# Kernel optimization log

Measured on AMD Instinct MI355X. Metric: run time of the kernel, lower is better.

The kernel has to match this reference:

```python
import jax, jax.numpy as jnp
import numpy as np

B, T, C, H, N, FF = 2, 1024, 2048, 32, 64, 8192
DIV = 8.0  # head_size_divisor
LAYER_ID, N_LAYER = 1, 24
EPS = 1e-5


def _layer_norm(x, g, b):
    m = x.mean(-1, keepdims=True)
    v = x.var(-1, keepdims=True)
    return (x - m) / jnp.sqrt(v + EPS) * g + b


def _group_norm(x, g, b):
    # GroupNorm(H, C) applied per token: normalize each head's N channels
    xg = x.reshape(B, T, H, N)
    m = xg.mean(-1, keepdims=True)
    v = xg.var(-1, keepdims=True)
    xn = ((xg - m) / jnp.sqrt(v + EPS)).reshape(B, T, C)
    return xn * g + b


def _time_shift(x):
    # xx[t] = x[t-1], xx[0] = 0
    return jnp.pad(x, ((0, 0), (1, 0), (0, 0)))[:, :-1]


def _wkv5(r, k, v, w, u):
    # r,k,v: [B,T,H,N]; w,u: [H,N]. Linear recurrence with per-channel decay.
    decay = jnp.exp(-jnp.exp(w))            # [H,N]
    dec = decay[None, :, :, None]           # broadcast over B and v-dim
    uu = u[None, :, :, None]
    rs = jnp.moveaxis(r, 1, 0)              # [T,B,H,N]
    ks = jnp.moveaxis(k, 1, 0)
    vs = jnp.moveaxis(v, 1, 0)

    def step(state, inp):                   # state: [B,H,N,N] (k-dim i, v-dim j)
        rt, kt, vt = inp
        kv = kt[..., :, None] * vt[..., None, :]          # [B,H,N,N]
        y = jnp.einsum('bhi,bhij->bhj', rt, uu * kv + state)
        return dec * state + kv, y

    state0 = jnp.zeros((B, H, N, N), r.dtype)
    _, ys = jax.lax.scan(step, state0, (rs, ks, vs))
    return jnp.moveaxis(ys, 0, 1).reshape(B, T, C)


def _forward(x, ln1_g, ln1_b, ln2_g, ln2_b,
             tm_k, tm_v, tm_r, tm_g, time_decay, time_faaaa,
             Wr, Wk, Wv, Wg, Wo, lnx_g, lnx_b,
             fm_k, fm_r, Wkey, Wrec, Wval):
    # ---- TimeMix ----
    xl = _layer_norm(x, ln1_g, ln1_b)
    xx = _time_shift(xl)
    xk = xl * tm_k + xx * (1 - tm_k)
    xv = xl * tm_v + xx * (1 - tm_v)
    xr = xl * tm_r + xx * (1 - tm_r)
    xg = xl * tm_g + xx * (1 - tm_g)
    r = (xr @ Wr).reshape(B, T, H, N)
    k = (xk @ Wk).reshape(B, T, H, N)
    v = (xv @ Wv).reshape(B, T, H, N)
    g = jax.nn.silu(xg @ Wg)
    att = _wkv5(r, k, v, time_decay, time_faaaa)
    att = _group_norm(att / DIV, lnx_g, lnx_b)
    x = x + (att * g) @ Wo
    # ---- ChannelMix ----
    xl2 = _layer_norm(x, ln2_g, ln2_b)
    xx2 = _time_shift(xl2)
    ck = xl2 * fm_k + xx2 * (1 - fm_k)
    cr = xl2 * fm_r + xx2 * (1 - fm_r)
    kk = jnp.square(jax.nn.relu(ck @ Wkey))
    kv = kk @ Wval
    return x + jax.nn.sigmoid(cr @ Wrec) * kv


def setup_inputs() -> dict:
    key = jax.random.key(0)
    ks = jax.random.split(key, 9)
    r01 = LAYER_ID / (N_LAYER - 1)
    r1a0 = 1.0 - LAYER_ID / N_LAYER
    ddd = (np.arange(C, dtype=np.float64) / C)[None, None, :]
    dec = np.array([-6 + 5 * (n / (C - 1)) ** (0.7 + 1.3 * r01) for n in range(C)])
    faa = np.array([r01 * (1 - n / (C - 1)) + ((n + 1) % 3 - 1) * 0.1 for n in range(C)])
    f32 = lambda a: jnp.asarray(a, jnp.float32)
    w = lambda k_, i, o: jax.random.normal(k_, (i, o), jnp.float32) * (i ** -0.5)
    return {
        'x': jax.random.normal(ks[0], (B, T, C), jnp.float32),
        'ln1_g': jnp.ones((C,), jnp.float32), 'ln1_b': jnp.zeros((C,), jnp.float32),
        'ln2_g': jnp.ones((C,), jnp.float32), 'ln2_b': jnp.zeros((C,), jnp.float32),
        'tm_k': f32(ddd ** r1a0), 'tm_v': f32(ddd ** r1a0 + 0.3 * r01),
        'tm_r': f32(ddd ** (0.5 * r1a0)), 'tm_g': f32(ddd ** (0.5 * r1a0)),
        'time_decay': f32(dec.reshape(H, N)), 'time_faaaa': f32(faa.reshape(H, N)),
        'Wr': w(ks[1], C, C), 'Wk': w(ks[2], C, C), 'Wv': w(ks[3], C, C),
        'Wg': w(ks[4], C, C), 'Wo': w(ks[5], C, C),
        'lnx_g': jnp.ones((C,), jnp.float32), 'lnx_b': jnp.zeros((C,), jnp.float32),
        'fm_k': f32(ddd ** r1a0), 'fm_r': f32(ddd ** r1a0),
        'Wkey': w(ks[6], C, FF), 'Wrec': w(ks[7], C, C), 'Wval': w(ks[8], FF, C),
    }


def reference(x, ln1_g, ln1_b, ln2_g, ln2_b,
              tm_k, tm_v, tm_r, tm_g, time_decay, time_faaaa,
              Wr, Wk, Wv, Wg, Wo, lnx_g, lnx_b,
              fm_k, fm_r, Wkey, Wrec, Wval):
    return _forward(x, ln1_g, ln1_b, ln2_g, ln2_b,
                    tm_k, tm_v, tm_r, tm_g, time_decay, time_faaaa,
                    Wr, Wk, Wv, Wg, Wo, lnx_g, lnx_b,
                    fm_k, fm_r, Wkey, Wrec, Wval)
```

## Files before the change

### kernel.cpp

```cpp
#include <hip/hip_runtime.h>
#include <stdint.h>

#define BB 2
#define TT 1024
#define CC 2048
#define HH 32
#define NNH 64
#define FFD 8192
#define MTOT (BB*TT)
#define LNEPS 1e-5f
#define LOG2E 1.44269504088896340736f

typedef __attribute__((ext_vector_type(8))) __bf16 bf16x8;
typedef __attribute__((ext_vector_type(4))) float f32x4;

#define USE_GLL 1
typedef __attribute__((address_space(1))) void GAS;
typedef __attribute__((address_space(3))) void LAS;

__device__ inline void gload_lds16(const uint16_t* g, uint16_t* l) {
#if USE_GLL
  __builtin_amdgcn_global_load_lds((GAS*)g, (LAS*)l, 16, 0, 0);
#else
  *(uint4*)l = *(const uint4*)g;
#endif
}

__device__ inline float bf2f(uint32_t u) {
  union { uint32_t i; float f; } v; v.i = u << 16; return v.f;
}
__device__ inline uint16_t f2bf(float f) {
  union { float f; uint32_t i; } v; v.f = f;
  uint32_t r = v.i + 0x7FFFu + ((v.i >> 16) & 1u);
  return (uint16_t)(r >> 16);
}
__device__ inline void unpack8(uint4 d, float* v) {
  v[0] = bf2f(d.x & 0xffffu); v[1] = bf2f(d.x >> 16);
  v[2] = bf2f(d.y & 0xffffu); v[3] = bf2f(d.y >> 16);
  v[4] = bf2f(d.z & 0xffffu); v[5] = bf2f(d.z >> 16);
  v[6] = bf2f(d.w & 0xffffu); v[7] = bf2f(d.w >> 16);
}
__device__ inline uint4 pack8(const float* v) {
  uint4 d;
  d.x = (uint32_t)f2bf(v[0]) | ((uint32_t)f2bf(v[1]) << 16);
  d.y = (uint32_t)f2bf(v[2]) | ((uint32_t)f2bf(v[3]) << 16);
  d.z = (uint32_t)f2bf(v[4]) | ((uint32_t)f2bf(v[5]) << 16);
  d.w = (uint32_t)f2bf(v[6]) | ((uint32_t)f2bf(v[7]) << 16);
  return d;
}

__device__ inline void load8f(const void* p, size_t idx, int fl, float* v) {
  if (fl) {
    const float* q = (const float*)p + idx;
    float4 a = *(const float4*)q; float4 b = *(const float4*)(q + 4);
    v[0]=a.x; v[1]=a.y; v[2]=a.z; v[3]=a.w; v[4]=b.x; v[5]=b.y; v[6]=b.z; v[7]=b.w;
  } else {
    unpack8(*(const uint4*)((const uint16_t*)p + idx), v);
  }
}
__device__ inline float load1f(const void* p, size_t idx, int fl) {
  return fl ? ((const float*)p)[idx] : bf2f(((const uint16_t*)p)[idx]);
}

__global__ void probe_kernel(const uint16_t* __restrict__ x, int* __restrict__ flag) {
  int tid = threadIdx.x;
  float m = 0.f;
  for (int i = tid; i < 4096; i += 64) {
    float a = fabsf(bf2f(x[i]));
    if (a > m) m = a;
  }
  for (int o = 32; o; o >>= 1) { float t = __shfl_down(m, o); if (t > m) m = t; }
  if (tid == 0) *flag = (m > 1e6f) ? 1 : 0;
}

template<int INMODE>
__global__ __launch_bounds__(256) void ln_kernel(const void* __restrict__ x,
    const void* __restrict__ g, const void* __restrict__ b,
    uint16_t* __restrict__ out, const int* __restrict__ dflag)
{
  int fl = *dflag;
  int row = blockIdx.x;
  int tid = threadIdx.x;
  int lane = tid & 63, wave = tid >> 6;
  size_t base = (size_t)row * CC + (size_t)tid * 8;
  float v[8];
  if constexpr (INMODE == 1) {
    const float* q = (const float*)x + base;
    float4 a = *(const float4*)q; float4 c = *(const float4*)(q + 4);
    v[0]=a.x; v[1]=a.y; v[2]=a.z; v[3]=a.w; v[4]=c.x; v[5]=c.y; v[6]=c.z; v[7]=c.w;
  } else {
    load8f(x, base, fl, v);
  }
  float s = 0.f, s2 = 0.f;
  #pragma unroll
  for (int j = 0; j < 8; j++) { s += v[j]; s2 += v[j] * v[j]; }
  for (int o = 32; o; o >>= 1) { s += __shfl_down(s, o); s2 += __shfl_down(s2, o); }
  __shared__ float red[8];
  if (lane == 0) { red[wave] = s; red[wave + 4] = s2; }
  __syncthreads();
  s  = red[0] + red[1] + red[2] + red[3];
  s2 = red[4] + red[5] + red[6] + red[7];
  float mean = s * (1.0f / CC);
  float var  = s2 * (1.0f / CC) - mean * mean;
  float rstd = rsqrtf(fmaxf(var, 0.f) + LNEPS);
  float gj[8], bj[8];
  load8f(g, (size_t)tid * 8, fl, gj);
  load8f(b, (size_t)tid * 8, fl, bj);
  float o8[8];
  #pragma unroll
  for (int j = 0; j < 8; j++) o8[j] = (v[j] - mean) * rstd * gj[j] + bj[j];
  *(uint4*)(out + base) = pack8(o8);
}

__global__ __launch_bounds__(256) void mix4_kernel(const uint16_t* __restrict__ xl,
    const void* __restrict__ tmr, const void* __restrict__ tmk,
    const void* __restrict__ tmv, const void* __restrict__ tmg,
    uint16_t* __restrict__ out, const int* __restrict__ dflag)
{
  int fl = *dflag;
  uint32_t idx = ((uint32_t)blockIdx.x * 256u + threadIdx.x) * 8u;
  uint32_t c = idx & (CC - 1);
  uint32_t row = idx >> 11;
  uint32_t t = row & (TT - 1);
  float xv[8], pv[8];
  unpack8(*(const uint4*)(xl + idx), xv);
  if (t) { unpack8(*(const uint4*)(xl + idx - CC), pv); }
  else   { for (int j = 0; j < 8; j++) pv[j] = 0.f; }
  const void* tms[4] = { tmr, tmk, tmv, tmg };
  const size_t SL = (size_t)MTOT * CC;
  #pragma unroll
  for (int a = 0; a < 4; a++) {
    float tm[8], o[8];
    load8f(tms[a], c, fl, tm);
    #pragma unroll
    for (int j = 0; j < 8; j++) o[j] = xv[j] * tm[j] + pv[j] * (1.f - tm[j]);
    *(uint4*)(out + a * SL + idx) = pack8(o);
  }
}

__global__ __launch_bounds__(256) void mix2_kernel(const uint16_t* __restrict__ xl,
    const void* __restrict__ tk, const void* __restrict__ tr,
    uint16_t* __restrict__ ok, uint16_t* __restrict__ orr,
    const int* __restrict__ dflag)
{
  int fl = *dflag;
  uint32_t idx = ((uint32_t)blockIdx.x * 256u + threadIdx.x) * 8u;
  uint32_t c = idx & (CC - 1);
  uint32_t row = idx >> 11;
  uint32_t t = row & (TT - 1);
  float xv[8], pv[8], tm[8], o[8];
  unpack8(*(const uint4*)(xl + idx), xv);
  if (t) { unpack8(*(const uint4*)(xl + idx - CC), pv); }
  else   { for (int j = 0; j < 8; j++) pv[j] = 0.f; }
  load8f(tk, c, fl, tm);
  #pragma unroll
  for (int j = 0; j < 8; j++) o[j] = xv[j] * tm[j] + pv[j] * (1.f - tm[j]);
  *(uint4*)(ok + idx) = pack8(o);
  load8f(tr, c, fl, tm);
  #pragma unroll
  for (int j = 0; j < 8; j++) o[j] = xv[j] * tm[j] + pv[j] * (1.f - tm[j]);
  *(uint4*)(orr + idx) = pack8(o);
}

__device__ inline void transpose_tile(const void* W, uint16_t* WT, int Kd, int Nd,
                                      int n0, int k0, int fl, int tid)
{
  __shared__ __align__(16) uint16_t tile[64][66];
  int r = tid >> 3, s = tid & 7;
  #pragma unroll
  for (int p = 0; p < 2; p++) {
    int row = p * 32 + r;
    float tv[8];
    load8f(W, (size_t)(k0 + row) * Nd + n0 + s * 8, fl, tv);
    uint16_t* t = &tile[row][s * 8];
    #pragma unroll
    for (int e = 0; e < 8; e++) t[e] = f2bf(tv[e]);
  }
  __syncthreads();
  #pragma unroll
  for (int p = 0; p < 2; p++) {
    int row = p * 32 + r;
    uint16_t tmp[8];
    #pragma unroll
    for (int e = 0; e < 8; e++) tmp[e] = tile[s * 8 + e][row];
    uint4 o;
    o.x = (uint32_t)tmp[0] | ((uint32_t)tmp[1] << 16);
    o.y = (uint32_t)tmp[2] | ((uint32_t)tmp[3] << 16);
    o.z = (uint32_t)tmp[4] | ((uint32_t)tmp[5] << 16);
    o.w = (uint32_t)tmp[6] | ((uint32_t)tmp[7] << 16);
    *(uint4*)(WT + (size_t)(n0 + row) * Kd + k0 + s * 8) = o;
  }
}

__global__ __launch_bounds__(256) void transpose_kernel(const void* __restrict__ W,
    uint16_t* __restrict__ WT, int Kd, int Nd, const int* __restrict__ dflag)
{
  transpose_tile(W, WT, Kd, Nd, blockIdx.x * 64, blockIdx.y * 64, *dflag, threadIdx.x);
}

__global__ __launch_bounds__(256) void transpose4_kernel(
    const void* __restrict__ W0, const void* __restrict__ W1,
    const void* __restrict__ W2, const void* __restrict__ W3,
    uint16_t* __restrict__ WT, const int* __restrict__ dflag)
{
  const void* Ws[4] = { W0, W1, W2, W3 };
  int z = blockIdx.z;
  transpose_tile(Ws[z], WT + (size_t)z * CC * CC, CC, CC,
                 blockIdx.x * 64, blockIdx.y * 64, *dflag, threadIdx.x);
}

enum { EPI_RESID = 2, EPI_RKVG = 6, EPI_FF2 = 7, EPI_PART = 8 };

template<int EPI>
__global__ __launch_bounds__(256, 2) void gemm_kernel(
    const uint16_t* __restrict__ Ain, const uint16_t* __restrict__ BTin,
    void* __restrict__ Cout, int N, int Kstride, int Kloop,
    const void* __restrict__ auxA, const float* __restrict__ auxf,
    const uint16_t* __restrict__ A2in, const uint16_t* __restrict__ BT2in,
    void* __restrict__ C2out, const int* __restrict__ dflag)
{
  const uint16_t* A  = Ain;
  const uint16_t* BT = BTin;
  uint16_t* co16 = (uint16_t*)Cout;
  float*    co32 = (float*)Cout;
  int fl = 0;
  if constexpr (EPI == EPI_RESID) fl = *dflag;
  bool silu = false, sigm = false;
  int bx = blockIdx.x;
  int N_ = N;
  int n0 = bx * 128;
  if constexpr (EPI == EPI_RKVG) {
    int z = blockIdx.z;
    A    += (size_t)z * MTOT * CC;
    BT   += (size_t)z * CC * CC;
    co16 += (size_t)z * MTOT * CC;
    silu = (z == 3);
  }
  if constexpr (EPI == EPI_PART) {
    int z = blockIdx.z;
    A    += (size_t)z * Kloop;
    BT   += (size_t)z * Kloop;
    co32 += (size_t)z * MTOT * 2048;
  }
  if constexpr (EPI == EPI_FF2) {
    if (bx >= 64) {
      n0 = (bx - 64) * 128;
      A = A2in; BT = BT2in; co16 = (uint16_t*)C2out; N_ = 2048; sigm = true;
    }
  }
  int m0 = blockIdx.y * 128;
  __shared__ __align__(16) uint16_t As[128 * 64];
  __shared__ __align__(16) uint16_t Bs[128 * 64];
  int tid = threadIdx.x;
  int lane = tid & 63, wave = tid >> 6;
  int wm = (wave >> 1) * 64, wn = (wave & 1) * 64;
  int l15 = lane & 15, lq = lane >> 4;
  int sw = l15 & 7;
  f32x4 acc[4][4];
  #pragma unroll
  for (int i = 0; i < 4; i++)
    #pragma unroll
    for (int j = 0; j < 4; j++) acc[i][j] = 0.f;
  const int rr = tid >> 3, seg = tid & 7;
  const int sseg = (seg ^ (rr & 7)) * 8;
  const uint16_t* Ag = A + (size_t)(m0 + rr) * Kstride + sseg;
  const uint16_t* Bg = BT + (size_t)(n0 + rr) * Kstride + sseg;
  uint16_t* Asw = As + tid * 8;
  uint16_t* Bsw = Bs + tid * 8;
  for (int k0 = 0; k0 < Kloop; k0 += 64) {
    __syncthreads();
    #pragma unroll
    for (int p = 0; p < 4; p++) {
      gload_lds16(Ag + (size_t)p * 32 * Kstride + k0, Asw + p * 2048);
      gload_lds16(Bg + (size_t)p * 32 * Kstride + k0, Bsw + p * 2048);
    }
    __syncthreads();
    #pragma unroll
    for (int kk = 0; kk < 2; kk++) {
      int cidx = ((kk * 4 + lq) ^ sw) * 8;
      bf16x8 af[4], bv[4];
      #pragma unroll
      for (int f = 0; f < 4; f++) af[f] = *(const bf16x8*)&As[(wm + f * 16 + l15) * 64 + cidx];
      #pragma unroll
      for (int f = 0; f < 4; f++) bv[f] = *(const bf16x8*)&Bs[(wn + f * 16 + l15) * 64 + cidx];
      #pragma unroll
      for (int fm = 0; fm < 4; fm++)
        #pragma unroll
        for (int fn = 0; fn < 4; fn++)
          acc[fm][fn] = __builtin_amdgcn_mfma_f32_16x16x32_bf16(af[fm], bv[fn], acc[fm][fn], 0, 0, 0);
    }
  }
  #pragma unroll
  for (int fm = 0; fm < 4; fm++) {
    #pragma unroll
    for (int q = 0; q < 4; q++) {
      int gr = m0 + wm + fm * 16 + lq * 4 + q;
      size_t rowb = (size_t)gr * N_;
      #pragma unroll
      for (int fn = 0; fn < 4; fn++) {
        int gc = n0 + wn + fn * 16 + l15;
        size_t idx = rowb + gc;
        float val = acc[fm][fn][q];
        if constexpr (EPI == EPI_RKVG) {
          if (silu) val = val / (1.f + __expf(-fmaxf(val, -80.f)));
          co16[idx] = f2bf(val);
        } else if constexpr (EPI == EPI_RESID) {
          co32[idx] = val + load1f(auxA, idx, fl);
        } else if constexpr (EPI == EPI_FF2) {
          if (sigm) {
            co16[idx] = f2bf(1.f / (1.f + __expf(-val)));
          } else {
            float t = fmaxf(val, 0.f);
            co16[idx] = f2bf(t * t);
          }
        } else if constexpr (EPI == EPI_PART) {
          co32[idx] = val;
        }
      }
    }
  }
}

__global__ __launch_bounds__(256) void final_reduce_kernel(
    const float* __restrict__ P, const float* __restrict__ x1,
    const uint16_t* __restrict__ sr, void* __restrict__ out,
    const int* __restrict__ dflag)
{
  int fl = *dflag;
  size_t idx = ((size_t)blockIdx.x * 256 + threadIdx.x) * 8;
  const float* P1 = P + (size_t)MTOT * 2048;
  float a[8], b[8], xv[8], s8[8], o[8];
  { float4 t0 = *(const float4*)(P + idx);  float4 t1 = *(const float4*)(P + idx + 4);
    a[0]=t0.x;a[1]=t0.y;a[2]=t0.z;a[3]=t0.w;a[4]=t1.x;a[5]=t1.y;a[6]=t1.z;a[7]=t1.w; }
  { float4 t0 = *(const float4*)(P1 + idx); float4 t1 = *(const float4*)(P1 + idx + 4);
    b[0]=t0.x;b[1]=t0.y;b[2]=t0.z;b[3]=t0.w;b[4]=t1.x;b[5]=t1.y;b[6]=t1.z;b[7]=t1.w; }
  { float4 t0 = *(const float4*)(x1 + idx); float4 t1 = *(const float4*)(x1 + idx + 4);
    xv[0]=t0.x;xv[1]=t0.y;xv[2]=t0.z;xv[3]=t0.w;xv[4]=t1.x;xv[5]=t1.y;xv[6]=t1.z;xv[7]=t1.w; }
  unpack8(*(const uint4*)(sr + idx), s8);
  #pragma unroll
  for (int j = 0; j < 8; j++) o[j] = xv[j] + s8[j] * (a[j] + b[j]);
  if (fl) {
    float* q = (float*)out + idx;
    *(float4*)q = make_float4(o[0], o[1], o[2], o[3]);
    *(float4*)(q + 4) = make_float4(o[4], o[5], o[6], o[7]);
  } else {
    *(uint4*)((uint16_t*)out + idx) = pack8(o);
  }
}

__global__ __launch_bounds__(256) void wkv_p_kernel(
    const uint16_t* __restrict__ kq, const uint16_t* __restrict__ vq,
    const void* __restrict__ wq, float* __restrict__ P,
    const int* __restrict__ dflag)
{
  int fl = *dflag;
  int blk = blockIdx.x;
  int c = blk & 15, h = (blk >> 4) & 31, b = blk >> 9;
  __shared__ __align__(16) float Kt[64][64];
  __shared__ __align__(16) uint16_t Vb[64][64];
  __shared__ __align__(16) float e_s[64];
  int tid = threadIdx.x;
  if (tid < 64) e_s[tid] = fminf(__expf(load1f(wq, h * 64 + tid, fl)), 100.f);
  __syncthreads();
  int rr = tid >> 3, cs = (tid & 7) * 8;
  #pragma unroll
  for (int p = 0; p < 2; p++) {
    int s = p * 32 + rr;
    size_t gbase = ((size_t)(b * TT + c * 64 + s)) * CC + h * 64 + cs;
    float k8[8];
    unpack8(*(const uint4*)(kq + gbase), k8);
    float sp = (float)(s + 1) * LOG2E;
    #pragma unroll
    for (int j = 0; j < 8; j++) Kt[s][cs + j] = k8[j] * exp2f(fminf(sp * e_s[cs + j], 80.f));
    *(uint4*)&Vb[s][cs] = *(const uint4*)(vq + gbase);
  }
  __syncthreads();
  int tx = tid & 15, ty = tid >> 4;
  int i0 = ty * 4, j0 = tx * 4;
  float acc[4][4] = {};
  for (int s = 0; s < 64; s++) {
    float4 a = *(const float4*)&Kt[s][i0];
    ushort4 vv = *(const ushort4*)&Vb[s][j0];
    float b0 = bf2f(vv.x), b1 = bf2f(vv.y), b2 = bf2f(vv.z), b3 = bf2f(vv.w);
    float am[4] = { a.x, a.y, a.z, a.w };
    #pragma unroll
    for (int m = 0; m < 4; m++) {
      acc[m][0] += am[m] * b0; acc[m][1] += am[m] * b1;
      acc[m][2] += am[m] * b2; acc[m][3] += am[m] * b3;
    }
  }
  float* Pb = P + (size_t)blk * 4096;
  #pragma unroll
  for (int m = 0; m < 4; m++) {
    float dl = exp2f(-64.0f * LOG2E * e_s[i0 + m]);
    float4 o = { acc[m][0] * dl, acc[m][1] * dl, acc[m][2] * dl, acc[m][3] * dl };
    *(float4*)&Pb[(i0 + m) * 64 + j0] = o;
  }
}

__global__ __launch_bounds__(256) void wkv_s_kernel(const float* __restrict__ P,
    const void* __restrict__ wq, float* __restrict__ S,
    const int* __restrict__ dflag)
{
  int fl = *dflag;
  int bh = blockIdx.x;
  int h = bh & 31;
  int tid = threadIdx.x;
  int i = tid >> 2, q = tid & 3;
  float e = fminf(__expf(load1f(wq, h * 64 + i, fl)), 100.f);
  float dl = exp2f(-64.0f * LOG2E * e);
  float4 s0 = {0,0,0,0}, s1 = {0,0,0,0}, s2 = {0,0,0,0}, s3 = {0,0,0,0};
  for (int c = 0; c < 16; c++) {
    size_t base = ((size_t)bh * 16 + c) * 4096 + (size_t)i * 64 + q * 16;
    *(float4*)&S[base + 0]  = s0;
    *(float4*)&S[base + 4]  = s1;
    *(float4*)&S[base + 8]  = s2;
    *(float4*)&S[base + 12] = s3;
    float4 p0 = *(const float4*)&P[base + 0];
    float4 p1 = *(const float4*)&P[base + 4];
    float4 p2 = *(const float4*)&P[base + 8];
    float4 p3 = *(const float4*)&P[base + 12];
    s0 = make_float4(dl * s0.x + p0.x, dl * s0.y + p0.y, dl * s0.z + p0.z, dl * s0.w + p0.w);
    s1 = make_float4(dl * s1.x + p1.x, dl * s1.y + p1.y, dl * s1.z + p1.z, dl * s1.w + p1.w);
    s2 = make_float4(dl * s2.x + p2.x, dl * s2.y + p2.y, dl * s2.z + p2.z, dl * s2.w + p2.w);
    s3 = make_float4(dl * s3.x + p3.x, dl * s3.y + p3.y, dl * s3.z + p3.z, dl * s3.w + p3.w);
  }
}

__global__ __launch_bounds__(256, 2) void wkv_y_kernel(
    const uint16_t* __restrict__ rq, const uint16_t* __restrict__ kq,
    const uint16_t* __restrict__ vq, const void* __restrict__ wq,
    const void* __restrict__ uq, const float* __restrict__ S,
    float* __restrict__ att, const int* __restrict__ dflag)
{
  int fl = *dflag;
  int blk = blockIdx.x;
  int c = blk & 15, h = (blk >> 4) & 31, b = blk >> 9;
  __shared__ __align__(16) float Rt[64][64];
  __shared__ __align__(16) float Kt[64][64];
  __shared__ __align__(16) uint16_t Vb[64][64];
  __shared__ __align__(16) float Ss[64][64];
  __shared__ __align__(16) float e_s[64];
  __shared__ __align__(16) float ud_s[64];
  int tid = threadIdx.x;
  if (tid < 64) {
    float e = fminf(__expf(load1f(wq, h * 64 + tid, fl)), 100.f);
    e_s[tid] = e;
    ud_s[tid] = load1f(uq, h * 64 + tid, fl) * __expf(-e);
  }
  __syncthreads();
  int rr = tid >> 3, cs = (tid & 7) * 8;
  #pragma unroll
  for (int p = 0; p < 2; p++) {
    int s = p * 32 + rr;
    size_t gbase = ((size_t)(b * TT + c * 64 + s)) * CC + h * 64 + cs;
    float r8[8], k8[8];
    unpack8(*(const uint4*)(rq + gbase), r8);
    unpack8(*(const uint4*)(kq + gbase), k8);
    float tneg = -(float)s * LOG2E;
    float spos = (float)(s + 1) * LOG2E;
    #pragma unroll
    for (int j = 0; j < 8; j++) {
      float e = e_s[cs + j];
      Rt[s][cs + j] = r8[j] * exp2f(tneg * e);
      Kt[s][cs + j] = k8[j] * exp2f(fminf(spos * e, 80.f));
    }
    *(uint4*)&Vb[s][cs] = *(const uint4*)(vq + gbase);
  }
  {
    int r2 = tid >> 2, q = tid & 3;
    const float* Sbp = S + (size_t)blk * 4096 + (size_t)r2 * 64 + q * 16;
    *(float4*)&Ss[r2][q * 16 + 0]  = *(const float4*)&Sbp[0];
    *(float4*)&Ss[r2][q * 16 + 4]  = *(const float4*)&Sbp[4];
    *(float4*)&Ss[r2][q * 16 + 8]  = *(const float4*)&Sbp[8];
    *(float4*)&Ss[r2][q * 16 + 12] = *(const float4*)&Sbp[12];
  }
  __syncthreads();
  int tx = tid & 15, ty = tid >> 4;
  int t0 = ty * 4, s0 = tx * 4;
  float acc[4][4] = {};
  for (int iq = 0; iq < 16; iq++) {
    int i = iq * 4;
    float4 ra[4], kb[4];
    #pragma unroll
    for (int m = 0; m < 4; m++) ra[m] = *(const float4*)&Rt[t0 + m][i];
    #pragma unroll
    for (int n = 0; n < 4; n++) kb[n] = *(const float4*)&Kt[s0 + n][i];
    #pragma unroll
    for (int m = 0; m < 4; m++)
      #pragma unroll
      for (int n = 0; n < 4; n++)
        acc[m][n] += ra[m].x * kb[n].x + ra[m].y * kb[n].y + ra[m].z * kb[n].z + ra[m].w * kb[n].w;
  }
  float dg = 0.f;
  if (tid < 64) {
    for (int iq = 0; iq < 16; iq++) {
      int i = iq * 4;
      float4 a = *(const float4*)&Rt[tid][i];
      float4 kk = *(const float4*)&Kt[tid][i];
      float4 u4 = *(const float4*)&ud_s[i];
      dg += a.x * kk.x * u4.x + a.y * kk.y * u4.y + a.z * kk.z * u4.z + a.w * kk.w * u4.w;
    }
  }
  __syncthreads();
  #pragma unroll
  for (int m = 0; m < 4; m++)
    #pragma unroll
    for (int n = 0; n < 4; n++) {
      int t = t0 + m, s = s0 + n;
      Kt[t][s] = (s < t) ? acc[m][n] : 0.0f;
    }
  __syncthreads();
  if (tid < 64) Kt[tid][tid] = dg;
  __syncthreads();
  int j0 = tx * 4;
  float y[4][4] = {};
  for (int sq = 0; sq < 16; sq++) {
    int s = sq * 4;
    float4 a4[4];
    #pragma unroll
    for (int m = 0; m < 4; m++) a4[m] = *(const float4*)&Kt[t0 + m][s];
    float vb[4][4];
    #pragma unroll
    for (int qq = 0; qq < 4; qq++) {
      ushort4 vv = *(const ushort4*)&Vb[s + qq][j0];
      vb[qq][0] = bf2f(vv.x); vb[qq][1] = bf2f(vv.y); vb[qq][2] = bf2f(vv.z); vb[qq][3] = bf2f(vv.w);
    }
    #pragma unroll
    for (int m = 0; m < 4; m++)
      #pragma unroll
      for (int n = 0; n < 4; n++)
        y[m][n] += a4[m].x * vb[0][n] + a4[m].y * vb[1][n] + a4[m].z * vb[2][n] + a4[m].w * vb[3][n];
  }
  for (int iq = 0; iq < 16; iq++) {
    int i = iq * 4;
    float4 r4[4], s4[4];
    #pragma unroll
    for (int m = 0; m < 4; m++) r4[m] = *(const float4*)&Rt[t0 + m][i];
    #pragma unroll
    for (int qq = 0; qq < 4; qq++) s4[qq] = *(const float4*)&Ss[i + qq][j0];
    #pragma unroll
    for (int m = 0; m < 4; m++)
      #pragma unroll
      for (int n = 0; n < 4; n++)
        y[m][n] += r4[m].x * s4[0][n] + r4[m].y * s4[1][n] + r4[m].z * s4[2][n] + r4[m].w * s4[3][n];
  }
  #pragma unroll
  for (int m = 0; m < 4; m++) {
    size_t ob = ((size_t)(b * TT + c * 64 + t0 + m)) * CC + h * 64 + j0;
    *(float4*)&att[ob] = make_float4(y[m][0], y[m][1], y[m][2], y[m][3]);
  }
}

__global__ __launch_bounds__(256) void gn_mul_kernel(const float* __restrict__ att,
    const void* __restrict__ gg, const void* __restrict__ bb,
    const uint16_t* __restrict__ gate, uint16_t* __restrict__ out,
    const int* __restrict__ dflag)
{
  int fl = *dflag;
  int row = blockIdx.x;
  int tid = threadIdx.x;
  size_t base = (size_t)row * CC + (size_t)tid * 8;
  float4 a0 = *(const float4*)(att + base);
  float4 a1 = *(const float4*)(att + base + 4);
  float v[8] = { a0.x, a0.y, a0.z, a0.w, a1.x, a1.y, a1.z, a1.w };
  #pragma unroll
  for (int j = 0; j < 8; j++) v[j] *= 0.125f;
  float s = 0.f, s2 = 0.f;
  #pragma unroll
  for (int j = 0; j < 8; j++) { s += v[j]; s2 += v[j] * v[j]; }
  s += __shfl_xor(s, 1); s += __shfl_xor(s, 2); s += __shfl_xor(s, 4);
  s2 += __shfl_xor(s2, 1); s2 += __shfl_xor(s2, 2); s2 += __shfl_xor(s2, 4);
  float m = s * (1.f / 64.f);
  float var = s2 * (1.f / 64.f) - m * m;
  float rstd = rsqrtf(fmaxf(var, 0.f) + LNEPS);
  int c = tid * 8;
  float g8[8], b8[8], gt8[8], o[8];
  load8f(gg, c, fl, g8);
  load8f(bb, c, fl, b8);
  unpack8(*(const uint4*)(gate + base), gt8);
  #pragma unroll
  for (int j = 0; j < 8; j++) o[j] = ((v[j] - m) * rstd * g8[j] + b8[j]) * gt8[j];
  *(uint4*)(out + base) = pack8(o);
}

extern "C" void kernel_launch(void* const* d_in, const int* in_sizes, int n_in,
                              void* d_out, int out_size, void* d_ws, size_t ws_size,
                              hipStream_t stream)
{
  const void* x    = d_in[0];
  const void* ln1g = d_in[1];
  const void* ln1b = d_in[2];
  const void* ln2g = d_in[3];
  const void* ln2b = d_in[4];
  const void* tmk  = d_in[5];
  const void* tmv  = d_in[6];
  const void* tmr  = d_in[7];
  const void* tmg  = d_in[8];
  const void* tdec = d_in[9];
  const void* tfaa = d_in[10];
  const void* Wr   = d_in[11];
  const void* Wk   = d_in[12];
  const void* Wv   = d_in[13];
  const void* Wg   = d_in[14];
  const void* Wo   = d_in[15];
  const void* lnxg = d_in[16];
  const void* lnxb = d_in[17];
  const void* fmk  = d_in[18];
  const void* fmr  = d_in[19];
  const void* Wkey = d_in[20];
  const void* Wrec = d_in[21];
  const void* Wval = d_in[22];

  char* ws = (char*)d_ws;
  const size_t SL  = (size_t)MTOT * CC;
  const size_t SLW = (size_t)CC * CC;
  uint16_t* XL    = (uint16_t*)(ws + 0);
  uint16_t* WRECT = XL;
  uint16_t* MIX4  = (uint16_t*)(ws + 8388608);
  float*    PART  = (float*)   (ws + 8388608);
  uint16_t* RKVG  = (uint16_t*)(ws + 41943040);
  float*    ATT   = (float*)   (ws + 75497472);
  float*    X1    = ATT;
  float*    Pb    = (float*)   (ws + 92274688);
  float*    Sb    = (float*)   (ws + 109051904);
  uint16_t* KK    = (uint16_t*)(ws + 92274688);
  uint16_t* WT    = (uint16_t*)(ws + 125829120);
  int*      FLAG  = (int*)     (ws + 159383552);
  (void)in_sizes; (void)n_in; (void)out_size; (void)ws_size;

  probe_kernel<<<dim3(1), 64, 0, stream>>>((const uint16_t*)x, FLAG);
  ln_kernel<0><<<dim3(MTOT), 256, 0, stream>>>(x, ln1g, ln1b, XL, FLAG);
  transpose4_kernel<<<dim3(32, 32, 4), 256, 0, stream>>>(Wr, Wk, Wv, Wg, WT, FLAG);
  mix4_kernel<<<dim3(2048), 256, 0, stream>>>(XL, tmr, tmk, tmv, tmg, MIX4, FLAG);
  gemm_kernel<EPI_RKVG><<<dim3(16, 16, 4), 256, 0, stream>>>(MIX4, WT, (void*)RKVG, CC, CC, CC,
      nullptr, nullptr, nullptr, nullptr, nullptr, FLAG);
  wkv_p_kernel<<<dim3(1024), 256, 0, stream>>>(RKVG + 1 * SL, RKVG + 2 * SL, tdec, Pb, FLAG);
  wkv_s_kernel<<<dim3(64), 256, 0, stream>>>(Pb, tdec, Sb, FLAG);
  wkv_y_kernel<<<dim3(1024), 256, 0, stream>>>(RKVG + 0 * SL, RKVG + 1 * SL, RKVG + 2 * SL, tdec, tfaa, Sb, ATT, FLAG);
  gn_mul_kernel<<<dim3(MTOT), 256, 0, stream>>>(ATT, lnxg, lnxb, RKVG + 3 * SL, MIX4, FLAG);
  transpose_kernel<<<dim3(32, 32), 256, 0, stream>>>(Wo, WT, CC, CC, FLAG);
  gemm_kernel<EPI_RESID><<<dim3(16, 16), 256, 0, stream>>>(MIX4, WT, (void*)X1, CC, CC, CC,
      x, nullptr, nullptr, nullptr, nullptr, FLAG);
  ln_kernel<1><<<dim3(MTOT), 256, 0, stream>>>(X1, ln2g, ln2b, XL, FLAG);
  mix2_kernel<<<dim3(2048), 256, 0, stream>>>(XL, fmk, fmr, MIX4, RKVG, FLAG);
  transpose_kernel<<<dim3(FFD / 64, CC / 64), 256, 0, stream>>>(Wkey, WT, CC, FFD, FLAG);
  transpose_kernel<<<dim3(32, 32), 256, 0, stream>>>(Wrec, WRECT, CC, CC, FLAG);
  gemm_kernel<EPI_FF2><<<dim3(80, 16), 256, 0, stream>>>(MIX4, WT, (void*)KK, FFD, CC, CC,
      nullptr, nullptr, RKVG, WRECT, (void*)(RKVG + 2 * SL), FLAG);
  transpose_kernel<<<dim3(CC / 64, FFD / 64), 256, 0, stream>>>(Wval, WT, FFD, CC, FLAG);
  gemm_kernel<EPI_PART><<<dim3(16, 16, 2), 256, 0, stream>>>(KK, WT, (void*)PART, CC, FFD, FFD / 2,
      nullptr, nullptr, nullptr, nullptr, nullptr, FLAG);
  final_reduce_kernel<<<dim3(2048), 256, 0, stream>>>(PART, X1, RKVG + 2 * SL, d_out, FLAG);
}
```

Before: 728.7 us.

## Fuse group-norm into WKV, split-K output GEMM, batch weight transposes

Group-norm and gating are folded into the wkv_y epilogue, so the fp32 ATT buffer and the gn_mul pass are gone. The Wo GEMM becomes a split-K partial GEMM, and a new ln2x kernel adds the partials plus the residual, writes X1 and runs LayerNorm2. When the workspace is large enough, all weight transposes are batched into two launches up front instead of interleaved launches. This cuts launches and fp32 round trips, but needs more workspace and adds a partial-sum buffer.

```diff
diff --git a/kernel.cpp b/kernel.cpp
--- a/kernel.cpp
+++ b/kernel.cpp
@@ -58,6 +58,15 @@
     unpack8(*(const uint4*)((const uint16_t*)p + idx), v);
   }
 }
+__device__ inline void load4f(const void* p, size_t idx, int fl, float* v) {
+  if (fl) {
+    float4 a = *(const float4*)((const float*)p + idx);
+    v[0]=a.x; v[1]=a.y; v[2]=a.z; v[3]=a.w;
+  } else {
+    ushort4 u = *(const ushort4*)((const uint16_t*)p + idx);
+    v[0]=bf2f(u.x); v[1]=bf2f(u.y); v[2]=bf2f(u.z); v[3]=bf2f(u.w);
+  }
+}
 __device__ inline float load1f(const void* p, size_t idx, int fl) {
   return fl ? ((const float*)p)[idx] : bf2f(((const uint16_t*)p)[idx]);
 }
@@ -73,7 +82,6 @@
   if (tid == 0) *flag = (m > 1e6f) ? 1 : 0;
 }
 
-template<int INMODE>
 __global__ __launch_bounds__(256) void ln_kernel(const void* __restrict__ x,
     const void* __restrict__ g, const void* __restrict__ b,
     uint16_t* __restrict__ out, const int* __restrict__ dflag)
@@ -84,13 +92,7 @@
   int lane = tid & 63, wave = tid >> 6;
   size_t base = (size_t)row * CC + (size_t)tid * 8;
   float v[8];
-  if constexpr (INMODE == 1) {
-    const float* q = (const float*)x + base;
-    float4 a = *(const float4*)q; float4 c = *(const float4*)(q + 4);
-    v[0]=a.x; v[1]=a.y; v[2]=a.z; v[3]=a.w; v[4]=c.x; v[5]=c.y; v[6]=c.z; v[7]=c.w;
-  } else {
-    load8f(x, base, fl, v);
-  }
+  load8f(x, base, fl, v);
   float s = 0.f, s2 = 0.f;
   #pragma unroll
   for (int j = 0; j < 8; j++) { s += v[j]; s2 += v[j] * v[j]; }
@@ -110,6 +112,48 @@
   #pragma unroll
   for (int j = 0; j < 8; j++) o8[j] = (v[j] - mean) * rstd * gj[j] + bj[j];
   *(uint4*)(out + base) = pack8(o8);
+}
+
+__global__ __launch_bounds__(256) void ln2x_kernel(const float* __restrict__ p0,
+    const void* __restrict__ x, const void* __restrict__ g, const void* __restrict__ b,
+    uint16_t* __restrict__ lnout, float* __restrict__ x1out,
+    const int* __restrict__ dflag)
+{
+  int fl = *dflag;
+  int row = blockIdx.x;
+  int tid = threadIdx.x;
+  int lane = tid & 63, wave = tid >> 6;
+  size_t base = (size_t)row * CC + (size_t)tid * 8;
+  const float* p1 = p0 + (size_t)MTOT * CC;
+  float v[8], xv[8];
+  { float4 a0 = *(const float4*)(p0 + base); float4 a1 = *(const float4*)(p0 + base + 4);
+    v[0]=a0.x; v[1]=a0.y; v[2]=a0.z; v[3]=a0.w; v[4]=a1.x; v[5]=a1.y; v[6]=a1.z; v[7]=a1.w; }
+  { float4 a0 = *(const float4*)(p1 + base); float4 a1 = *(const float4*)(p1 + base + 4);
+    v[0]+=a0.x; v[1]+=a0.y; v[2]+=a0.z; v[3]+=a0.w; v[4]+=a1.x; v[5]+=a1.y; v[6]+=a1.z; v[7]+=a1.w; }
+  load8f(x, base, fl, xv);
+  #pragma unroll
+  for (int j = 0; j < 8; j++) v[j] += xv[j];
+  *(float4*)(x1out + base)     = make_float4(v[0], v[1], v[2], v[3]);
+  *(float4*)(x1out + base + 4) = make_float4(v[4], v[5], v[6], v[7]);
+  float s = 0.f, s2 = 0.f;
+  #pragma unroll
+  for (int j = 0; j < 8; j++) { s += v[j]; s2 += v[j] * v[j]; }
+  for (int o = 32; o; o >>= 1) { s += __shfl_down(s, o); s2 += __shfl_down(s2, o); }
+  __shared__ float red[8];
+  if (lane == 0) { red[wave] = s; red[wave + 4] = s2; }
+  __syncthreads();
+  s  = red[0] + red[1] + red[2] + red[3];
+  s2 = red[4] + red[5] + red[6] + red[7];
+  float mean = s * (1.0f / CC);
+  float var  = s2 * (1.0f / CC) - mean * mean;
+  float rstd = rsqrtf(fmaxf(var, 0.f) + LNEPS);
+  float gj[8], bj[8];
+  load8f(g, (size_t)tid * 8, fl, gj);
+  load8f(b, (size_t)tid * 8, fl, bj);
+  float o8[8];
+  #pragma unroll
+  for (int j = 0; j < 8; j++) o8[j] = (v[j] - mean) * rstd * gj[j] + bj[j];
+  *(uint4*)(lnout + base) = pack8(o8);
 }
 
 __global__ __launch_bounds__(256) void mix4_kernel(const uint16_t* __restrict__ xl,
@@ -209,13 +253,36 @@
                  blockIdx.x * 64, blockIdx.y * 64, *dflag, threadIdx.x);
 }
 
-enum { EPI_RESID = 2, EPI_RKVG = 6, EPI_FF2 = 7, EPI_PART = 8 };
+__global__ __launch_bounds__(256) void transpose6_kernel(
+    const void* __restrict__ W0, const void* __restrict__ W1,
+    const void* __restrict__ W2, const void* __restrict__ W3,
+    const void* __restrict__ W4, const void* __restrict__ W5,
+    uint16_t* __restrict__ WT, const int* __restrict__ dflag)
+{
+  const void* Ws[6] = { W0, W1, W2, W3, W4, W5 };
+  int z = blockIdx.z;
+  transpose_tile(Ws[z], WT + (size_t)z * CC * CC, CC, CC,
+                 blockIdx.x * 64, blockIdx.y * 64, *dflag, threadIdx.x);
+}
+
+__global__ __launch_bounds__(256) void transpose_rect2_kernel(
+    const void* __restrict__ Wkey, const void* __restrict__ Wval,
+    uint16_t* __restrict__ WTkey, uint16_t* __restrict__ WTval,
+    const int* __restrict__ dflag)
+{
+  int fl = *dflag;
+  if (blockIdx.z == 0)
+    transpose_tile(Wkey, WTkey, CC, FFD, blockIdx.x * 64, blockIdx.y * 64, fl, threadIdx.x);
+  else
+    transpose_tile(Wval, WTval, FFD, CC, blockIdx.y * 64, blockIdx.x * 64, fl, threadIdx.x);
+}
+
+enum { EPI_RKVG = 6, EPI_FF2 = 7, EPI_PART = 8 };
 
 template<int EPI>
 __global__ __launch_bounds__(256, 2) void gemm_kernel(
     const uint16_t* __restrict__ Ain, const uint16_t* __restrict__ BTin,
     void* __restrict__ Cout, int N, int Kstride, int Kloop,
-    const void* __restrict__ auxA, const float* __restrict__ auxf,
     const uint16_t* __restrict__ A2in, const uint16_t* __restrict__ BT2in,
     void* __restrict__ C2out, const int* __restrict__ dflag)
 {
@@ -223,8 +290,6 @@
   const uint16_t* BT = BTin;
   uint16_t* co16 = (uint16_t*)Cout;
   float*    co32 = (float*)Cout;
-  int fl = 0;
-  if constexpr (EPI == EPI_RESID) fl = *dflag;
   bool silu = false, sigm = false;
   int bx = blockIdx.x;
   int N_ = N;
@@ -304,8 +369,6 @@
         if constexpr (EPI == EPI_RKVG) {
           if (silu) val = val / (1.f + __expf(-fmaxf(val, -80.f)));
           co16[idx] = f2bf(val);
-        } else if constexpr (EPI == EPI_RESID) {
-          co32[idx] = val + load1f(auxA, idx, fl);
         } else if constexpr (EPI == EPI_FF2) {
           if (sigm) {
             co16[idx] = f2bf(1.f / (1.f + __expf(-val)));
@@ -431,7 +494,9 @@
     const uint16_t* __restrict__ rq, const uint16_t* __restrict__ kq,
     const uint16_t* __restrict__ vq, const void* __restrict__ wq,
     const void* __restrict__ uq, const float* __restrict__ S,
-    float* __restrict__ att, const int* __restrict__ dflag)
+    const void* __restrict__ lnxg, const void* __restrict__ lnxb,
+    const uint16_t* __restrict__ gate, uint16_t* __restrict__ outp,
+    const int* __restrict__ dflag)
 {
   int fl = *dflag;
   int blk = blockIdx.x;
@@ -545,43 +610,36 @@
       for (int n = 0; n < 4; n++)
         y[m][n] += r4[m].x * s4[0][n] + r4[m].y * s4[1][n] + r4[m].z * s4[2][n] + r4[m].w * s4[3][n];
   }
+  float g4[4], b4[4];
+  load4f(lnxg, (size_t)h * 64 + j0, fl, g4);
+  load4f(lnxb, (size_t)h * 64 + j0, fl, b4);
   #pragma unroll
   for (int m = 0; m < 4; m++) {
-    size_t ob = ((size_t)(b * TT + c * 64 + t0 + m)) * CC + h * 64 + j0;
-    *(float4*)&att[ob] = make_float4(y[m][0], y[m][1], y[m][2], y[m][3]);
-  }
-}
-
-__global__ __launch_bounds__(256) void gn_mul_kernel(const float* __restrict__ att,
-    const void* __restrict__ gg, const void* __restrict__ bb,
-    const uint16_t* __restrict__ gate, uint16_t* __restrict__ out,
-    const int* __restrict__ dflag)
-{
-  int fl = *dflag;
-  int row = blockIdx.x;
-  int tid = threadIdx.x;
-  size_t base = (size_t)row * CC + (size_t)tid * 8;
-  float4 a0 = *(const float4*)(att + base);
-  float4 a1 = *(const float4*)(att + base + 4);
-  float v[8] = { a0.x, a0.y, a0.z, a0.w, a1.x, a1.y, a1.z, a1.w };
-  #pragma unroll
-  for (int j = 0; j < 8; j++) v[j] *= 0.125f;
-  float s = 0.f, s2 = 0.f;
-  #pragma unroll
-  for (int j = 0; j < 8; j++) { s += v[j]; s2 += v[j] * v[j]; }
-  s += __shfl_xor(s, 1); s += __shfl_xor(s, 2); s += __shfl_xor(s, 4);
-  s2 += __shfl_xor(s2, 1); s2 += __shfl_xor(s2, 2); s2 += __shfl_xor(s2, 4);
-  float m = s * (1.f / 64.f);
-  float var = s2 * (1.f / 64.f) - m * m;
-  float rstd = rsqrtf(fmaxf(var, 0.f) + LNEPS);
-  int c = tid * 8;
-  float g8[8], b8[8], gt8[8], o[8];
-  load8f(gg, c, fl, g8);
-  load8f(bb, c, fl, b8);
-  unpack8(*(const uint4*)(gate + base), gt8);
-  #pragma unroll
-  for (int j = 0; j < 8; j++) o[j] = ((v[j] - m) * rstd * g8[j] + b8[j]) * gt8[j];
-  *(uint4*)(out + base) = pack8(o);
+    float s = 0.f, s2 = 0.f;
+    #pragma unroll
+    for (int n = 0; n < 4; n++) {
+      float v = y[m][n] * 0.125f;
+      s += v; s2 += v * v;
+    }
+    s += __shfl_xor(s, 1); s2 += __shfl_xor(s2, 1);
+    s += __shfl_xor(s, 2); s2 += __shfl_xor(s2, 2);
+    s += __shfl_xor(s, 4); s2 += __shfl_xor(s2, 4);
+    s += __shfl_xor(s, 8); s2 += __shfl_xor(s2, 8);
+    float mean = s * (1.f / 64.f);
+    float var  = s2 * (1.f / 64.f) - mean * mean;
+    float rstd = rsqrtf(fmaxf(var, 0.f) + LNEPS);
+    size_t rb = ((size_t)(b * TT + c * 64 + t0 + m)) * CC + h * 64 + j0;
+    ushort4 gv = *(const ushort4*)&gate[rb];
+    float gt[4] = { bf2f(gv.x), bf2f(gv.y), bf2f(gv.z), bf2f(gv.w) };
+    uint2 pk;
+    float o0 = ((y[m][0] * 0.125f - mean) * rstd * g4[0] + b4[0]) * gt[0];
+    float o1 = ((y[m][1] * 0.125f - mean) * rstd * g4[1] + b4[1]) * gt[1];
+    float o2 = ((y[m][2] * 0.125f - mean) * rstd * g4[2] + b4[2]) * gt[2];
+    float o3 = ((y[m][3] * 0.125f - mean) * rstd * g4[3] + b4[3]) * gt[3];
+    pk.x = (uint32_t)f2bf(o0) | ((uint32_t)f2bf(o1) << 16);
+    pk.y = (uint32_t)f2bf(o2) | ((uint32_t)f2bf(o3) << 16);
+    *(uint2*)&outp[rb] = pk;
+  }
 }
 
 extern "C" void kernel_launch(void* const* d_in, const int* in_sizes, int n_in,
@@ -611,45 +669,65 @@
   const void* Wkey = d_in[20];
   const void* Wrec = d_in[21];
   const void* Wval = d_in[22];
+  (void)in_sizes; (void)n_in; (void)out_size;
 
   char* ws = (char*)d_ws;
+  const size_t MB = 1024 * 1024;
   const size_t SL  = (size_t)MTOT * CC;
   const size_t SLW = (size_t)CC * CC;
   uint16_t* XL    = (uint16_t*)(ws + 0);
-  uint16_t* WRECT = XL;
-  uint16_t* MIX4  = (uint16_t*)(ws + 8388608);
-  float*    PART  = (float*)   (ws + 8388608);
-  uint16_t* RKVG  = (uint16_t*)(ws + 41943040);
-  float*    ATT   = (float*)   (ws + 75497472);
-  float*    X1    = ATT;
-  float*    Pb    = (float*)   (ws + 92274688);
-  float*    Sb    = (float*)   (ws + 109051904);
-  uint16_t* KK    = (uint16_t*)(ws + 92274688);
-  uint16_t* WT    = (uint16_t*)(ws + 125829120);
-  int*      FLAG  = (int*)     (ws + 159383552);
-  (void)in_sizes; (void)n_in; (void)out_size; (void)ws_size;
+  uint16_t* MIX4  = (uint16_t*)(ws + 8 * MB);
+  float*    PART  = (float*)   (ws + 8 * MB);
+  uint16_t* RKVG  = (uint16_t*)(ws + 40 * MB);
+  float*    X1    = (float*)   (ws + 72 * MB);
+  float*    Pb    = (float*)   (ws + 88 * MB);
+  float*    Sb    = (float*)   (ws + 104 * MB);
+  float*    RPART = (float*)   (ws + 88 * MB);
+  uint16_t* KK    = (uint16_t*)(ws + 88 * MB);
+  uint16_t* WT    = (uint16_t*)(ws + 120 * MB);
+
+  const bool big = ws_size >= 233 * MB + 4096;
+  int* FLAG = (int*)(ws + (big ? 232 * MB : 152 * MB));
 
   probe_kernel<<<dim3(1), 64, 0, stream>>>((const uint16_t*)x, FLAG);
-  ln_kernel<0><<<dim3(MTOT), 256, 0, stream>>>(x, ln1g, ln1b, XL, FLAG);
-  transpose4_kernel<<<dim3(32, 32, 4), 256, 0, stream>>>(Wr, Wk, Wv, Wg, WT, FLAG);
+  ln_kernel<<<dim3(MTOT), 256, 0, stream>>>(x, ln1g, ln1b, XL, FLAG);
+
+  const uint16_t *WT_RKVG, *WT_WO, *WT_WREC, *WT_WKEY, *WT_WVAL;
+  if (big) {
+    WT_RKVG = WT;
+    WT_WO   = WT + 4 * SLW;
+    WT_WREC = WT + 5 * SLW;
+    WT_WKEY = WT + 6 * SLW;
+    WT_WVAL = WT + 6 * SLW + (size_t)CC * FFD;
+    transpose6_kernel<<<dim3(32, 32, 6), 256, 0, stream>>>(Wr, Wk, Wv, Wg, Wo, Wrec, WT, FLAG);
+    transpose_rect2_kernel<<<dim3(128, 32, 2), 256, 0, stream>>>(Wkey, Wval,
+        (uint16_t*)WT_WKEY, (uint16_t*)WT_WVAL, FLAG);
+  } else {
+    WT_RKVG = WT; WT_WO = WT; WT_WREC = XL ; WT_WKEY = WT; WT_WVAL = WT;
+    transpose4_kernel<<<dim3(32, 32, 4), 256, 0, stream>>>(Wr, Wk, Wv, Wg, WT, FLAG);
+  }
+
   mix4_kernel<<<dim3(2048), 256, 0, stream>>>(XL, tmr, tmk, tmv, tmg, MIX4, FLAG);
-  gemm_kernel<EPI_RKVG><<<dim3(16, 16, 4), 256, 0, stream>>>(MIX4, WT, (void*)RKVG, CC, CC, CC,
-      nullptr, nullptr, nullptr, nullptr, nullptr, FLAG);
+  gemm_kernel<EPI_RKVG><<<dim3(16, 16, 4), 256, 0, stream>>>(MIX4, WT_RKVG, (void*)RKVG,
+      CC, CC, CC, nullptr, nullptr, nullptr, FLAG);
   wkv_p_kernel<<<dim3(1024), 256, 0, stream>>>(RKVG + 1 * SL, RKVG + 2 * SL, tdec, Pb, FLAG);
   wkv_s_kernel<<<dim3(64), 256, 0, stream>>>(Pb, tdec, Sb, FLAG);
-  wkv_y_kernel<<<dim3(1024), 256, 0, stream>>>(RKVG + 0 * SL, RKVG + 1 * SL, RKVG + 2 * SL, tdec, tfaa, Sb, ATT, FLAG);
-  gn_mul_kernel<<<dim3(MTOT), 256, 0, stream>>>(ATT, lnxg, lnxb, RKVG + 3 * SL, MIX4, FLAG);
-  transpose_kernel<<<dim3(32, 32), 256, 0, stream>>>(Wo, WT, CC, CC, FLAG);
-  gemm_kernel<EPI_RESID><<<dim3(16, 16), 256, 0, stream>>>(MIX4, WT, (void*)X1, CC, CC, CC,
-      x, nullptr, nullptr, nullptr, nullptr, FLAG);
-  ln_kernel<1><<<dim3(MTOT), 256, 0, stream>>>(X1, ln2g, ln2b, XL, FLAG);
+  wkv_y_kernel<<<dim3(1024), 256, 0, stream>>>(RKVG + 0 * SL, RKVG + 1 * SL, RKVG + 2 * SL,
+      tdec, tfaa, Sb, lnxg, lnxb, RKVG + 3 * SL, MIX4, FLAG);
+  if (!big) transpose_kernel<<<dim3(32, 32), 256, 0, stream>>>(Wo, WT, CC, CC, FLAG);
+  gemm_kernel<EPI_PART><<<dim3(16, 16, 2), 256, 0, stream>>>(MIX4, WT_WO, (void*)RPART,
+      CC, CC, CC / 2, nullptr, nullptr, nullptr, FLAG);
+  ln2x_kernel<<<dim3(MTOT), 256, 0, stream>>>(RPART, x, ln2g, ln2b, XL, X1, FLAG);
   mix2_kernel<<<dim3(2048), 256, 0, stream>>>(XL, fmk, fmr, MIX4, RKVG, FLAG);
-  transpose_kernel<<<dim3(FFD / 64, CC / 64), 256, 0, stream>>>(Wkey, WT, CC, FFD, FLAG);
-  transpose_kernel<<<dim3(32, 32), 256, 0, stream>>>(Wrec, WRECT, CC, CC, FLAG);
-  gemm_kernel<EPI_FF2><<<dim3(80, 16), 256, 0, stream>>>(MIX4, WT, (void*)KK, FFD, CC, CC,
-      nullptr, nullptr, RKVG, WRECT, (void*)(RKVG + 2 * SL), FLAG);
-  transpose_kernel<<<dim3(CC / 64, FFD / 64), 256, 0, stream>>>(Wval, WT, FFD, CC, FLAG);
-  gemm_kernel<EPI_PART><<<dim3(16, 16, 2), 256, 0, stream>>>(KK, WT, (void*)PART, CC, FFD, FFD / 2,
-      nullptr, nullptr, nullptr, nullptr, nullptr, FLAG);
+  if (!big) {
+    transpose_kernel<<<dim3(FFD / 64, CC / 64), 256, 0, stream>>>(Wkey, WT, CC, FFD, FLAG);
+    transpose_kernel<<<dim3(32, 32), 256, 0, stream>>>(Wrec, XL, CC, CC, FLAG);
+    WT_WREC = XL;
+  }
+  gemm_kernel<EPI_FF2><<<dim3(80, 16), 256, 0, stream>>>(MIX4, WT_WKEY, (void*)KK,
+      FFD, CC, CC, RKVG, WT_WREC, (void*)(RKVG + 2 * SL), FLAG);
+  if (!big) transpose_kernel<<<dim3(CC / 64, FFD / 64), 256, 0, stream>>>(Wval, WT, FFD, CC, FLAG);
+  gemm_kernel<EPI_PART><<<dim3(16, 16, 2), 256, 0, stream>>>(KK, WT_WVAL, (void*)PART,
+      CC, FFD, FFD / 2, nullptr, nullptr, nullptr, FLAG);
   final_reduce_kernel<<<dim3(2048), 256, 0, stream>>>(PART, X1, RKVG + 2 * SL, d_out, FLAG);
 }
```

Measured after the change: 729.3 us. Within noise of the previous version (+0.1%).
